# Kernel optimization log

Hardware: AMD Instinct MI355X
Metric: run time of the kernel (lower is better)

The kernel has to match this reference:

```python
import jax, jax.numpy as jnp
import numpy as np
import math

B, S, DIM = 1, 2048, 4096
N_HEADS, N_KV, HEAD_DIM = 32, 8, 128
WINDOW = 2048
ROPE_THETA = 10000.0


def setup_inputs() -> dict:
    key = jax.random.key(0)
    ks = jax.random.split(key, 6)
    w_std = 0.02
    x = jax.random.normal(ks[0], (B, S, DIM), dtype=jnp.float32)
    wq = jax.random.normal(ks[1], (DIM, N_HEADS * HEAD_DIM), dtype=jnp.float32) * w_std
    wk = jax.random.normal(ks[2], (DIM, N_KV * HEAD_DIM), dtype=jnp.float32) * w_std
    wv = jax.random.normal(ks[3], (DIM, N_KV * HEAD_DIM), dtype=jnp.float32) * w_std
    wo = jax.random.normal(ks[4], (N_HEADS * HEAD_DIM, DIM), dtype=jnp.float32) * w_std
    # rotary tables (real/imag of complex_rotary_matrix)
    pos = jnp.arange(S, dtype=jnp.float32)
    inv_freq = 1.0 / (ROPE_THETA ** (jnp.arange(0, HEAD_DIM, 2, dtype=jnp.float32) / HEAD_DIM))
    angles = pos[:, None] * inv_freq[None, :]  # [S, HEAD_DIM/2]
    cos, sin = jnp.cos(angles), jnp.sin(angles)
    positions = jnp.arange(S, dtype=jnp.int32)
    # sliding-window causal additive mask: allow j <= i and i - j < WINDOW
    i = jnp.arange(S)[:, None]
    j = jnp.arange(S)[None, :]
    allowed = (j <= i) & (i - j < WINDOW)
    mask = jnp.where(allowed, 0.0, -jnp.inf).astype(jnp.float32)
    cache_k = jnp.zeros((B, WINDOW, N_KV, HEAD_DIM), dtype=jnp.float32)
    cache_v = jnp.zeros((B, WINDOW, N_KV, HEAD_DIM), dtype=jnp.float32)
    return dict(x=x, wq=wq, wk=wk, wv=wv, wo=wo, cos=cos, sin=sin,
                positions=positions, mask=mask, cache_k=cache_k, cache_v=cache_v)


def _apply_rope(t, cos, sin):
    # t: [B, S, H, D]; interleaved complex pairs as in torch.view_as_complex
    tp = t.reshape(*t.shape[:-1], HEAD_DIM // 2, 2)
    te, to = tp[..., 0], tp[..., 1]
    c = cos[None, :, None, :]
    s = sin[None, :, None, :]
    re = te * c - to * s
    im = te * s + to * c
    return jnp.stack([re, im], axis=-1).reshape(t.shape)


def reference(x, wq, wk, wv, wo, cos, sin, positions, mask, cache_k, cache_v):
    repeats = N_HEADS // N_KV
    q = (x @ wq).reshape(B, S, N_HEADS, HEAD_DIM)
    k = (x @ wk).reshape(B, S, N_KV, HEAD_DIM)
    v = (x @ wv).reshape(B, S, N_KV, HEAD_DIM)
    q = _apply_rope(q, cos, sin)
    k = _apply_rope(k, cos, sin)
    # rolling KV-cache scatter update (prefill path: positions.shape[0] > 1)
    scatter_pos = positions[-WINDOW:] % WINDOW
    new_cache_k = cache_k.at[:, scatter_pos].set(k[:, -WINDOW:])
    new_cache_v = cache_v.at[:, scatter_pos].set(v[:, -WINDOW:])
    # GQA head repetition (repeat_kv_head)
    k = jnp.repeat(k, repeats, axis=2)  # [B, S, N_HEADS, D]
    v = jnp.repeat(v, repeats, axis=2)
    scores = jnp.einsum('bqhd,bkhd->bhqk', q, k) / math.sqrt(HEAD_DIM)
    scores = scores + mask[None, None, :, :]
    attn = jax.nn.softmax(scores.astype(jnp.float32), axis=-1).astype(q.dtype)
    out = jnp.einsum('bhqk,bkhd->bqhd', attn, v)
    out = out.reshape(B, S, N_HEADS * HEAD_DIM)
    return out @ wo, new_cache_k, new_cache_v
```

## Files before the change

kernel.cpp:

```cpp
#include <hip/hip_runtime.h>

typedef __bf16 bf16;
typedef __bf16 bf16x8 __attribute__((ext_vector_type(8)));
typedef __bf16 bf16x4 __attribute__((ext_vector_type(4)));
typedef float  f32x4  __attribute__((ext_vector_type(4)));

__device__ __forceinline__ f32x4 mfma16(bf16x8 a, bf16x8 b, f32x4 c) {
  return __builtin_amdgcn_mfma_f32_16x16x32_bf16(a, b, c, 0, 0, 0);
}

__device__ __forceinline__ void gload16(const bf16* g, bf16* l) {
  __builtin_amdgcn_global_load_lds(
      (const __attribute__((address_space(1))) void*)g,
      (__attribute__((address_space(3))) void*)l, 16, 0, 0);
}

__global__ void cast_x_kernel(const float* __restrict__ in, bf16* __restrict__ out) {
  const int i = blockIdx.x * 256 + threadIdx.x;
  const float4 v = ((const float4*)in)[i];
  bf16x4 o;
  o[0] = (bf16)v.x; o[1] = (bf16)v.y; o[2] = (bf16)v.z; o[3] = (bf16)v.w;
  *(bf16x4*)&out[(size_t)i * 4] = o;
}

__global__ void transpose_cast(const float* __restrict__ in, bf16* __restrict__ out,
                               int ldin, int ldout) {
  __shared__ bf16 t[32][33];
  const int c0 = blockIdx.x * 32, r0 = blockIdx.y * 32;
  const int x = threadIdx.x, y = threadIdx.y;
  #pragma unroll
  for (int i = 0; i < 32; i += 8)
    t[y + i][x] = (bf16)in[(size_t)(r0 + y + i) * ldin + c0 + x];
  __syncthreads();
  #pragma unroll
  for (int i = 0; i < 32; i += 8)
    out[(size_t)(c0 + y + i) * ldout + r0 + x] = t[x][y + i];
}

__global__ void permute_v(const bf16* __restrict__ qkv, bf16* __restrict__ vp) {
  __shared__ bf16 t[32][33];
  const int sb  = blockIdx.x;
  const int kvh = blockIdx.y >> 2;
  const int dt  = blockIdx.y & 3;
  const int x = threadIdx.x, y = threadIdx.y;
  #pragma unroll
  for (int i = 0; i < 32; i += 8)
    t[y + i][x] = qkv[(size_t)(sb * 32 + y + i) * 6144 + 5120 + kvh * 128 + dt * 32 + x];
  __syncthreads();
  #pragma unroll
  for (int i = 0; i < 32; i += 8)
    vp[((size_t)(kvh * 64 + sb) * 128 + dt * 32 + y + i) * 32 + x] = t[x][y + i];
}

#define MMQ(MB, NB)                                                            \
  _Pragma("unroll")                                                            \
  for (int mi = 0; mi < 4; ++mi)                                               \
    _Pragma("unroll")                                                          \
    for (int ni = 0; ni < 2; ++ni)                                             \
      _Pragma("unroll")                                                        \
      for (int kk = 0; kk < 2; ++kk)                                           \
        acc[MB + mi][NB + ni] =                                                \
            mfma16(ar[mi][kk], br[NB + ni][kk], acc[MB + mi][NB + ni]);

#define PH_OPEN                                                                \
  __builtin_amdgcn_s_barrier();                                                \
  asm volatile("s_waitcnt lgkmcnt(0)" ::: "memory");                           \
  __builtin_amdgcn_s_setprio(1);

#define PH_CLOSE                                                               \
  __builtin_amdgcn_s_setprio(0);                                               \
  __builtin_amdgcn_s_barrier();

template <typename OutT>
__global__ __launch_bounds__(512, 2)
void gemm8(const bf16* __restrict__ A, const bf16* __restrict__ Bt,
           OutT* __restrict__ C, int M, int N, int K, int ldc) {
  __shared__ __attribute__((aligned(16))) bf16 lds[65536];
  char* ldsc = (char*)lds;
  constexpr int AO0 = 0, BO0 = 32768, AO1 = 65536, BO1 = 98304;

  const int t    = threadIdx.x;
  const int w    = t >> 6;
  const int lane = t & 63;
  const int l15  = lane & 15;
  const int lg   = lane >> 4;
  const int wm   = w >> 2;
  const int wn   = w & 3;
  const int hb   = wn >> 1;
  const int bm   = (blockIdx.x & 7) * 256;
  const int bn   = (blockIdx.x >> 3) * 256;

  const int d0     = t * 16;
  const int dsw    = d0 ^ (((d0 >> 9) & 1) << 5);
  const int srow_s = (dsw >> 6) & 127;
  const int scol_e = (dsw & 63) >> 1;

  auto stg = [&](const bf16* P, int rowbase, int tile, int half, int region) {
    const bf16* s = P + (size_t)(rowbase + half * 128 + srow_s) * K + tile * 64 + scol_e;
    gload16(s,      (bf16*)(ldsc + region + half * 16384 + w * 1024));
    gload16(s + 32, (bf16*)(ldsc + region + half * 16384 + 8192 + w * 1024));
  };
  auto lda = [&](int AO, int m, int kk) -> bf16x8 {
    int byte = AO + wm * 16384 + kk * 8192 + (m * 16 + l15) * 64 + lg * 16;
    byte ^= ((byte >> 9) & 1) << 5;
    return *(const bf16x8*)(ldsc + byte);
  };
  auto ldb = [&](int BO, int n, int kk) -> bf16x8 {
    int byte = BO + hb * 16384 + kk * 8192 +
               ((wn & 1) * 64 + n * 16 + l15) * 64 + lg * 16;
    byte ^= ((byte >> 9) & 1) << 5;
    return *(const bf16x8*)(ldsc + byte);
  };

  f32x4 acc[8][4] = {};
  bf16x8 ar[4][2], br[4][2];

  const int NT = K >> 6;
  const int NI = K >> 7;

  stg(A,  bm, 0, 0, AO0);  stg(A,  bm, 0, 1, AO0);
  stg(Bt, bn, 0, 0, BO0);  stg(Bt, bn, 0, 1, BO0);
  stg(Bt, bn, 1, 0, BO1);  stg(Bt, bn, 1, 1, BO1);
  asm volatile("s_waitcnt vmcnt(4)" ::: "memory");
  __builtin_amdgcn_s_barrier();

  #pragma unroll 1
  for (int it = 0; it < NI; ++it) {
    const int t1 = 2 * it + 1;
    const int t2 = (2 * it + 2 < NT) ? 2 * it + 2 : NT - 1;
    const int t3 = (2 * it + 3 < NT) ? 2 * it + 3 : NT - 1;

    #pragma unroll
    for (int mi = 0; mi < 4; ++mi) {
      ar[mi][0] = lda(AO0, mi, 0); ar[mi][1] = lda(AO0, mi, 1);
    }
    #pragma unroll
    for (int ni = 0; ni < 2; ++ni) {
      br[ni][0] = ldb(BO0, ni, 0); br[ni][1] = ldb(BO0, ni, 1);
    }
    stg(A, bm, t1, 0, AO1);
    PH_OPEN; MMQ(0, 0); PH_CLOSE;
    #pragma unroll
    for (int ni = 2; ni < 4; ++ni) {
      br[ni][0] = ldb(BO0, ni, 0); br[ni][1] = ldb(BO0, ni, 1);
    }
    stg(A, bm, t1, 1, AO1);
    PH_OPEN; MMQ(0, 2); PH_CLOSE;
    #pragma unroll
    for (int mi = 0; mi < 4; ++mi) {
      ar[mi][0] = lda(AO0, 4 + mi, 0); ar[mi][1] = lda(AO0, 4 + mi, 1);
    }
    stg(Bt, bn, t2, 0, BO0);
    PH_OPEN; MMQ(4, 0); PH_CLOSE;
    stg(Bt, bn, t2, 1, BO0);
    PH_OPEN; MMQ(4, 2);
    __builtin_amdgcn_s_setprio(0);
    asm volatile("s_waitcnt vmcnt(4)" ::: "memory");
    __builtin_amdgcn_s_barrier();
    #pragma unroll
    for (int mi = 0; mi < 4; ++mi) {
      ar[mi][0] = lda(AO1, mi, 0); ar[mi][1] = lda(AO1, mi, 1);
    }
    #pragma unroll
    for (int ni = 0; ni < 2; ++ni) {
      br[ni][0] = ldb(BO1, ni, 0); br[ni][1] = ldb(BO1, ni, 1);
    }
    stg(A, bm, t2, 0, AO0);
    PH_OPEN; MMQ(0, 0); PH_CLOSE;
    #pragma unroll
    for (int ni = 2; ni < 4; ++ni) {
      br[ni][0] = ldb(BO1, ni, 0); br[ni][1] = ldb(BO1, ni, 1);
    }
    stg(A, bm, t2, 1, AO0);
    PH_OPEN; MMQ(0, 2); PH_CLOSE;
    #pragma unroll
    for (int mi = 0; mi < 4; ++mi) {
      ar[mi][0] = lda(AO1, 4 + mi, 0); ar[mi][1] = lda(AO1, 4 + mi, 1);
    }
    stg(Bt, bn, t3, 0, BO1);
    PH_OPEN; MMQ(4, 0); PH_CLOSE;
    stg(Bt, bn, t3, 1, BO1);
    PH_OPEN; MMQ(4, 2);
    __builtin_amdgcn_s_setprio(0);
    asm volatile("s_waitcnt vmcnt(4)" ::: "memory");
    __builtin_amdgcn_s_barrier();
  }

  #pragma unroll
  for (int mi = 0; mi < 8; ++mi)
    #pragma unroll
    for (int ni = 0; ni < 4; ++ni)
      #pragma unroll
      for (int rr = 0; rr < 4; ++rr)
        C[(size_t)(bm + wm * 128 + mi * 16 + lg * 4 + rr) * ldc +
          (bn + wn * 64 + ni * 16 + l15)] = (OutT)acc[mi][ni][rr];
}

__global__ void rope_q_kernel(bf16* __restrict__ q, const float* __restrict__ cs,
                              const float* __restrict__ sn) {
  const int idx = blockIdx.x * 256 + threadIdx.x;
  const int p  = idx & 63;
  const int sh = idx >> 6;
  const int h  = sh & 31;
  const int s  = sh >> 5;
  const float c  = cs[s * 64 + p];
  const float si = sn[s * 64 + p];
  const size_t ii = (size_t)s * 6144 + h * 128 + 2 * p;
  const float te = (float)q[ii], to = (float)q[ii + 1];
  q[ii]     = (bf16)(te * c - to * si);
  q[ii + 1] = (bf16)(te * si + to * c);
}

__global__ void rope_k_kernel(const bf16* __restrict__ qkv, bf16* __restrict__ kp,
                              float* __restrict__ ck, const float* __restrict__ cs,
                              const float* __restrict__ sn) {
  const int idx = blockIdx.x * 256 + threadIdx.x;
  const int p  = idx & 63;
  const int sh = idx >> 6;
  const int h  = sh & 7;
  const int s  = sh >> 3;
  const float c  = cs[s * 64 + p];
  const float si = sn[s * 64 + p];
  const size_t ii = (size_t)s * 6144 + 4096 + h * 128 + 2 * p;
  const float te = (float)qkv[ii], to = (float)qkv[ii + 1];
  const float re = te * c - to * si;
  const float im = te * si + to * c;
  const size_t io = ((size_t)(h * 4 + (p >> 4)) * 2048 + s) * 32 + ((2 * p) & 31);
  kp[io]     = (bf16)re;
  kp[io + 1] = (bf16)im;
  const size_t ic = (size_t)s * 1024 + h * 128 + 2 * p;
  ck[ic]     = re;
  ck[ic + 1] = im;
}

__global__ void cast_v_kernel(const bf16* __restrict__ qkv, float* __restrict__ cv) {
  const int i = blockIdx.x * 256 + threadIdx.x;
  const int s = i >> 8;
  const int c = (i & 255) * 4;
  const bf16x4 v = *(const bf16x4*)&qkv[(size_t)s * 6144 + 5120 + c];
  float4 o;
  o.x = (float)v[0]; o.y = (float)v[1]; o.z = (float)v[2]; o.w = (float)v[3];
  *(float4*)&cv[(size_t)s * 1024 + c] = o;
}

__global__ __launch_bounds__(256, 3)
void attn_fwd(const bf16* __restrict__ Q, const bf16* __restrict__ Kp,
              const bf16* __restrict__ Vp, bf16* __restrict__ O) {
  __shared__ __attribute__((aligned(16))) bf16 Kb[8192];
  __shared__ __attribute__((aligned(16))) bf16 Vb[8192];
  __shared__ __attribute__((aligned(16))) bf16 P_lds[4][16][72];
  const int id   = blockIdx.x;
  const int qt   = 31 - (id >> 5);
  const int kvh  = id & 7;
  const int sub  = (id >> 3) & 3;
  const int h    = kvh * 4 + sub;
  const int t    = threadIdx.x;
  const int w    = t >> 6;
  const int lane = t & 63;
  const int l15  = lane & 15;
  const int lg   = lane >> 4;
  const float scale = 0.08838834764831845f;
  const bf16* Kh = Kp + (size_t)kvh * 262144;
  const bf16* Vh = Vp + (size_t)kvh * 262144;
  const int koff = (t >> 2) * 32 + (t & 3) * 8;

  const int qw  = qt * 64 + w * 16;
  const int myq = qw + l15;

  bf16x8 qf[4];
  #pragma unroll
  for (int ds = 0; ds < 4; ++ds)
    qf[ds] = *(const bf16x8*)&Q[(size_t)myq * 6144 + h * 128 + ds * 32 + lg * 8];

  f32x4 o[8] = {};
  float m = -1e30f, ell = 0.f;

  #pragma unroll
  for (int i = 0; i < 4; ++i)
    gload16(Kh + (size_t)i * 65536 + koff, Kb + i * 2048 + w * 512);
  #pragma unroll
  for (int i = 0; i < 4; ++i)
    gload16(Vh + (size_t)i * 2048 + koff, Vb + i * 2048 + w * 512);
  __syncthreads();

  #pragma unroll 1
  for (int kt = 0; kt <= qt; ++kt) {
    f32x4 T[4] = {};
    __builtin_amdgcn_s_setprio(1);
    #pragma unroll
    for (int kb = 0; kb < 4; ++kb)
      #pragma unroll
      for (int ds = 0; ds < 4; ++ds) {
        bf16x8 kf = *(const bf16x8*)&Kb[(ds * 64 + kb * 16 + l15) * 32 + lg * 8];
        T[kb] = mfma16(kf, qf[ds], T[kb]);
      }
    __builtin_amdgcn_s_setprio(0);
    __syncthreads();
    if (kt < qt) {
      #pragma unroll
      for (int i = 0; i < 4; ++i)
        gload16(Kh + (size_t)i * 65536 + (kt + 1) * 2048 + koff,
                Kb + i * 2048 + w * 512);
    }

    float pv[16];
    float pmax = -1e30f;
    if (kt == qt) {
      #pragma unroll
      for (int kb = 0; kb < 4; ++kb)
        #pragma unroll
        for (int r = 0; r < 4; ++r) {
          const int key = qt * 64 + kb * 16 + lg * 4 + r;
          const float s = (key > myq) ? -1e30f : T[kb][r] * scale;
          pv[kb * 4 + r] = s;
          pmax = fmaxf(pmax, s);
        }
    } else {
      #pragma unroll
      for (int kb = 0; kb < 4; ++kb)
        #pragma unroll
        for (int r = 0; r < 4; ++r) {
          const float s = T[kb][r] * scale;
          pv[kb * 4 + r] = s;
          pmax = fmaxf(pmax, s);
        }
    }
    float base = m;
    if (!__all(pmax - m <= 8.f)) {
      float wmax = pmax;
      wmax = fmaxf(wmax, __shfl_xor(wmax, 16));
      wmax = fmaxf(wmax, __shfl_xor(wmax, 32));
      const float newm = fmaxf(m, wmax);
      const float corr = __expf(m - newm);
      ell *= corr;
      m = newm; base = newm;
      float sf[4];
      #pragma unroll
      for (int r = 0; r < 4; ++r) sf[r] = __shfl(corr, lg * 4 + r);
      #pragma unroll
      for (int df = 0; df < 8; ++df)
        #pragma unroll
        for (int r = 0; r < 4; ++r) o[df][r] *= sf[r];
    }
    bf16 pb[16];
    float tsum = 0.f;
    #pragma unroll
    for (int i = 0; i < 16; ++i) {
      const float p = __expf(pv[i] - base);
      tsum += p;
      pb[i] = (bf16)p;
    }
    ell += tsum;

    #pragma unroll
    for (int kb = 0; kb < 4; ++kb) {
      bf16x4 pk;
      pk[0] = pb[kb * 4 + 0]; pk[1] = pb[kb * 4 + 1];
      pk[2] = pb[kb * 4 + 2]; pk[3] = pb[kb * 4 + 3];
      *(bf16x4*)&P_lds[w][l15][kb * 16 + lg * 4] = pk;
    }
    __builtin_amdgcn_s_setprio(1);
    #pragma unroll
    for (int ks = 0; ks < 2; ++ks) {
      bf16x8 pa = *(const bf16x8*)&P_lds[w][l15][ks * 32 + lg * 8];
      #pragma unroll
      for (int df = 0; df < 8; ++df) {
        bf16x8 vf = *(const bf16x8*)&Vb[(ks * 128 + df * 16 + l15) * 32 + lg * 8];
        o[df] = mfma16(pa, vf, o[df]);
      }
    }
    __builtin_amdgcn_s_setprio(0);
    __syncthreads();
    if (kt < qt) {
      #pragma unroll
      for (int i = 0; i < 4; ++i)
        gload16(Vh + (size_t)(kt + 1) * 8192 + i * 2048 + koff,
                Vb + i * 2048 + w * 512);
    }
  }

  ell += __shfl_xor(ell, 16);
  ell += __shfl_xor(ell, 32);
  float er[4];
  #pragma unroll
  for (int r = 0; r < 4; ++r) er[r] = 1.f / __shfl(ell, lg * 4 + r);
  #pragma unroll
  for (int df = 0; df < 8; ++df)
    #pragma unroll
    for (int r = 0; r < 4; ++r)
      O[(size_t)(qw + lg * 4 + r) * 4096 + h * 128 + df * 16 + l15] =
          (bf16)(o[df][r] * er[r]);
}

extern "C" void kernel_launch(void* const* d_in, const int* in_sizes, int n_in,
                              void* d_out, int out_size, void* d_ws, size_t ws_size,
                              hipStream_t stream) {
  const float* x    = (const float*)d_in[0];
  const float* wq   = (const float*)d_in[1];
  const float* wk   = (const float*)d_in[2];
  const float* wv   = (const float*)d_in[3];
  const float* wo   = (const float*)d_in[4];
  const float* cosf_ = (const float*)d_in[5];
  const float* sinf_ = (const float*)d_in[6];

  float* out     = (float*)d_out;
  float* cache_k = out + (size_t)8388608;
  float* cache_v = cache_k + (size_t)2097152;
  bf16* qkv = (bf16*)d_out;

  bf16* ws = (bf16*)d_ws;
  bf16* wT = ws;
  bf16* kp = ws + (size_t)25165824;
  bf16* vp = kp + (size_t)2097152;
  bf16* xb = vp + (size_t)2097152;
  bf16* aout = xb;

  const dim3 tb(32, 8);
  cast_x_kernel<<<8192, 256, 0, stream>>>(x, xb);
  transpose_cast<<<dim3(128, 128), tb, 0, stream>>>(wq, wT, 4096, 4096);
  transpose_cast<<<dim3(32, 128), tb, 0, stream>>>(wk, wT + (size_t)16777216,
                                                   1024, 4096);
  transpose_cast<<<dim3(32, 128), tb, 0, stream>>>(wv, wT + (size_t)20971520,
                                                   1024, 4096);
  gemm8<bf16><<<192, 512, 0, stream>>>(xb, wT, qkv, 2048, 6144, 4096, 6144);
  rope_q_kernel<<<16384, 256, 0, stream>>>(qkv, cosf_, sinf_);
  rope_k_kernel<<<4096, 256, 0, stream>>>(qkv, kp, cache_k, cosf_, sinf_);
  cast_v_kernel<<<2048, 256, 0, stream>>>(qkv, cache_v);
  permute_v<<<dim3(64, 32), tb, 0, stream>>>(qkv, vp);
  transpose_cast<<<dim3(128, 128), tb, 0, stream>>>(wo, wT, 4096, 4096);
  attn_fwd<<<1024, 256, 0, stream>>>(qkv, kp, vp, aout);
  gemm8<float><<<128, 512, 0, stream>>>(aout, wT, out, 2048, 4096, 4096, 4096);
}
```

Before: 362.2 us.

## Split-K the output projection GEMM into two halves with a reduce kernel

Adds a template split-K parameter to the GEMM with a remapped block-to-tile index. The output projection now launches 256 blocks, each covering half of K, instead of 128 blocks. Each half writes bf16 partials to workspace, and a new kernel sums them into the fp32 output. This fills more of the GPU's compute units for the final GEMM, at the cost of an extra kernel launch, partial-buffer traffic, and bf16 rounding of the partial sums.

```diff
diff --git a/kernel.cpp b/kernel.cpp
--- a/kernel.cpp
+++ b/kernel.cpp
@@ -71,10 +71,11 @@
   __builtin_amdgcn_s_setprio(0);                                               \
   __builtin_amdgcn_s_barrier();
 
-template <typename OutT>
+template <typename OutT, int NSPLIT>
 __global__ __launch_bounds__(512, 2)
 void gemm8(const bf16* __restrict__ A, const bf16* __restrict__ Bt,
-           OutT* __restrict__ C, int M, int N, int K, int ldc) {
+           OutT* __restrict__ C0, OutT* __restrict__ C1,
+           int M, int N, int K, int ldc) {
   __shared__ __attribute__((aligned(16))) bf16 lds[65536];
   char* ldsc = (char*)lds;
   constexpr int AO0 = 0, BO0 = 32768, AO1 = 65536, BO1 = 98304;
@@ -87,8 +88,18 @@
   const int wm   = w >> 2;
   const int wn   = w & 3;
   const int hb   = wn >> 1;
-  const int bm   = (blockIdx.x & 7) * 256;
-  const int bn   = (blockIdx.x >> 3) * 256;
+
+  const int nbm = M >> 8;
+  const int nb2 = nbm * NSPLIT;
+  const int cpx = (nb2 * (N >> 8)) >> 3;
+  const int lid = ((int)blockIdx.x & 7) * cpx + ((int)blockIdx.x >> 3);
+  const int bn  = (lid / nb2) * 256;
+  const int rem = lid % nb2;
+  const int kh  = rem / nbm;
+  const int bm  = (rem % nbm) * 256;
+  const int Kloc = K / NSPLIT;
+  const int koff = kh * Kloc;
+  OutT* __restrict__ C = (NSPLIT == 2 && kh) ? C1 : C0;
 
   const int d0     = t * 16;
   const int dsw    = d0 ^ (((d0 >> 9) & 1) << 5);
@@ -96,7 +107,8 @@
   const int scol_e = (dsw & 63) >> 1;
 
   auto stg = [&](const bf16* P, int rowbase, int tile, int half, int region) {
-    const bf16* s = P + (size_t)(rowbase + half * 128 + srow_s) * K + tile * 64 + scol_e;
+    const bf16* s = P + (size_t)(rowbase + half * 128 + srow_s) * K +
+                    koff + tile * 64 + scol_e;
     gload16(s,      (bf16*)(ldsc + region + half * 16384 + w * 1024));
     gload16(s + 32, (bf16*)(ldsc + region + half * 16384 + 8192 + w * 1024));
   };
@@ -115,8 +127,8 @@
   f32x4 acc[8][4] = {};
   bf16x8 ar[4][2], br[4][2];
 
-  const int NT = K >> 6;
-  const int NI = K >> 7;
+  const int NT = Kloc >> 6;
+  const int NI = Kloc >> 7;
 
   stg(A,  bm, 0, 0, AO0);  stg(A,  bm, 0, 1, AO0);
   stg(Bt, bn, 0, 0, BO0);  stg(Bt, bn, 0, 1, BO0);
@@ -194,6 +206,19 @@
       for (int rr = 0; rr < 4; ++rr)
         C[(size_t)(bm + wm * 128 + mi * 16 + lg * 4 + rr) * ldc +
           (bn + wn * 64 + ni * 16 + l15)] = (OutT)acc[mi][ni][rr];
+}
+
+__global__ void reduce_out(const bf16* __restrict__ p0, const bf16* __restrict__ p1,
+                           float* __restrict__ out) {
+  const int i = blockIdx.x * 256 + threadIdx.x;
+  const bf16x4 a = *(const bf16x4*)&p0[(size_t)i * 4];
+  const bf16x4 b = *(const bf16x4*)&p1[(size_t)i * 4];
+  float4 o;
+  o.x = (float)a[0] + (float)b[0];
+  o.y = (float)a[1] + (float)b[1];
+  o.z = (float)a[2] + (float)b[2];
+  o.w = (float)a[3] + (float)b[3];
+  *(float4*)&out[(size_t)i * 4] = o;
 }
 
 __global__ void rope_q_kernel(bf16* __restrict__ q, const float* __restrict__ cs,
@@ -414,6 +439,8 @@
   bf16* vp = kp + (size_t)2097152;
   bf16* xb = vp + (size_t)2097152;
   bf16* aout = xb;
+  bf16* part1 = wT + (size_t)16777216;
+  bf16* part0 = ws + (size_t)37748736;
 
   const dim3 tb(32, 8);
   cast_x_kernel<<<8192, 256, 0, stream>>>(x, xb);
@@ -422,12 +449,14 @@
                                                    1024, 4096);
   transpose_cast<<<dim3(32, 128), tb, 0, stream>>>(wv, wT + (size_t)20971520,
                                                    1024, 4096);
-  gemm8<bf16><<<192, 512, 0, stream>>>(xb, wT, qkv, 2048, 6144, 4096, 6144);
+  gemm8<bf16, 1><<<192, 512, 0, stream>>>(xb, wT, qkv, qkv, 2048, 6144, 4096, 6144);
   rope_q_kernel<<<16384, 256, 0, stream>>>(qkv, cosf_, sinf_);
   rope_k_kernel<<<4096, 256, 0, stream>>>(qkv, kp, cache_k, cosf_, sinf_);
   cast_v_kernel<<<2048, 256, 0, stream>>>(qkv, cache_v);
   permute_v<<<dim3(64, 32), tb, 0, stream>>>(qkv, vp);
   transpose_cast<<<dim3(128, 128), tb, 0, stream>>>(wo, wT, 4096, 4096);
   attn_fwd<<<1024, 256, 0, stream>>>(qkv, kp, vp, aout);
-  gemm8<float><<<128, 512, 0, stream>>>(aout, wT, out, 2048, 4096, 4096, 4096);
-}
+  gemm8<bf16, 2><<<256, 512, 0, stream>>>(aout, wT, part0, part1,
+                                          2048, 4096, 4096, 4096);
+  reduce_out<<<8192, 256, 0, stream>>>(part0, part1, out);
+}
```

Result: faster. 329.3 us, median of 2 (-9.1%).
